# Performance work log

Measured on AMD Instinct MI355X. Metric: run time of the kernel, lower is better.

## Reference

```python
import jax, jax.numpy as jnp
import numpy as np

H = 16   # heads
M = 4    # stride / number of sparse slices


def setup_inputs() -> dict:
    key = jax.random.key(0)
    ks = jax.random.split(key, 5)
    B, L, D = 4, 4096, 1024
    s = 0.02
    return {
        "x": jax.random.normal(ks[0], (B, L, D), dtype=jnp.float32),
        "Wq": jax.random.normal(ks[1], (D, D), dtype=jnp.float32) * s,
        "bq": jnp.zeros((D,), dtype=jnp.float32),
        "Wk": jax.random.normal(ks[2], (D, D), dtype=jnp.float32) * s,
        "bk": jnp.zeros((D,), dtype=jnp.float32),
        "Wv": jax.random.normal(ks[3], (D, D), dtype=jnp.float32) * s,
        "bv": jnp.zeros((D,), dtype=jnp.float32),
        "Wo": jax.random.normal(ks[4], (D, D), dtype=jnp.float32) * s,
        "bo": jnp.zeros((D,), dtype=jnp.float32),
    }


def _strided_heads(y, B, L, D):
    # y: [B, L, D] -> [B, H, M, n, d_k] where slice m holds tokens m, m+M, m+2M, ...
    dk = D // H
    n = L // M
    y = y.reshape(B, L, H, dk).transpose(0, 2, 1, 3)          # [B,H,L,dk]
    y = y.reshape(B, H, n, M, dk).transpose(0, 1, 3, 2, 4)    # [B,H,M,n,dk]
    return y


def reference(x, Wq, bq, Wk, bk, Wv, bv, Wo, bo):
    B, L, D = x.shape
    dk = D // H
    n = L // M
    # projections (PyTorch Linear math: x @ W + b with W stored as [in, out] here)
    q = _strided_heads(x @ Wq + bq, B, L, D)   # [B,H,M,n,dk]
    k = _strided_heads(x @ Wk + bk, B, L, D)
    v = _strided_heads(x @ Wv + bv, B, L, D)
    # per-slice attention over the n strided tokens of each of the M slices
    scores = jnp.einsum("bhmqd,bhmkd->bhmqk", q, k) / jnp.sqrt(jnp.float32(dk))
    p = jax.nn.softmax(scores, axis=-1)
    o = jnp.einsum("bhmqk,bhmkd->bhmqd", p, v)                # [B,H,M,n,dk]
    # scatter back: slice m writes positions m::M  ==  interleave m and n dims
    o = o.transpose(0, 1, 3, 2, 4).reshape(B, H, L, dk)       # [B,H,L,dk]
    o = o.transpose(0, 2, 1, 3).reshape(B, L, D)              # [B,L,D]
    return o @ Wo + bo
```

## Files before the change

kernel.cpp:

```cpp
#include <hip/hip_runtime.h>
#include <hip/hip_bf16.h>


typedef __attribute__((ext_vector_type(8))) short short8;
typedef __attribute__((ext_vector_type(8))) unsigned short ushort8v;
typedef __attribute__((ext_vector_type(4))) float floatx4;

__device__ __forceinline__ float b2f(unsigned short h) {
    union { unsigned int u; float f; } v; v.u = ((unsigned int)h) << 16; return v.f;
}
__device__ __forceinline__ unsigned short f2b(float f) {
    union { float f; unsigned int u; } v; v.f = f;
    unsigned int r = v.u + 0x7fffu + ((v.u >> 16) & 1u);
    return (unsigned short)(r >> 16);
}
__device__ __forceinline__ unsigned int pack2bf(float lo, float hi) {
    union { float f; unsigned int u; } a, b; a.f = lo; b.f = hi;
    return ((b.u + 0x8000u) & 0xFFFF0000u) | (((a.u + 0x8000u) >> 16) & 0xFFFFu);
}
__device__ __forceinline__ void async_copy16(const unsigned short* g, unsigned short* l) {
    __builtin_amdgcn_global_load_lds((const __attribute__((address_space(1))) void*)g,
                                     (__attribute__((address_space(3))) void*)l, 16, 0, 0);
}

__global__ __launch_bounds__(256)
void cvt_kernel(const float* __restrict__ in, unsigned short* __restrict__ out, int n4) {
    int i = blockIdx.x * 256 + threadIdx.x;
    if (i >= n4) return;
    float4 v = ((const float4*)in)[i];
    ushort4 o;
    o.x = f2b(v.x); o.y = f2b(v.y); o.z = f2b(v.z); o.w = f2b(v.w);
    ((ushort4*)out)[i] = o;
}

__global__ __launch_bounds__(256)
void cvt_w_t(const float* __restrict__ Wq, const float* __restrict__ Wk,
             const float* __restrict__ Wv, const float* __restrict__ Wo,
             unsigned short* __restrict__ Wt3, unsigned short* __restrict__ Wot, float s0) {
    __shared__ float tile[64][65];
    const int kt = blockIdx.x, nt = blockIdx.y, z = blockIdx.z;
    const float* W = (z == 0) ? Wq : (z == 1) ? Wk : (z == 2) ? Wv : Wo;
    unsigned short* Wt = (z < 3) ? (Wt3 + (size_t)z * 1048576) : Wot;
    const float sc = (z == 0) ? s0 : 1.0f;
    const int t = threadIdx.x;
    const int r = t >> 2, cg = t & 3;
    const float* src = W + (size_t)(kt * 64 + r) * 1024 + nt * 64 + cg * 16;
#pragma unroll
    for (int j = 0; j < 4; j++) {
        float4 v = *(const float4*)(src + j * 4);
        tile[r][cg * 16 + j * 4 + 0] = v.x;
        tile[r][cg * 16 + j * 4 + 1] = v.y;
        tile[r][cg * 16 + j * 4 + 2] = v.z;
        tile[r][cg * 16 + j * 4 + 3] = v.w;
    }
    __syncthreads();
    unsigned short* dst = Wt + (size_t)(nt * 64 + r) * 1024 + kt * 64 + cg * 16;
    ushort8v o0, o1;
#pragma unroll
    for (int j = 0; j < 8; j++) o0[j] = f2b(tile[cg * 16 + j][r] * sc);
#pragma unroll
    for (int j = 0; j < 8; j++) o1[j] = f2b(tile[cg * 16 + 8 + j][r] * sc);
    *(ushort8v*)(dst) = o0;
    *(ushort8v*)(dst + 8) = o1;
}

template <bool F32OUT>
__global__ __launch_bounds__(256, 2)
void gemm_k(const unsigned short* __restrict__ A,
            const unsigned short* __restrict__ BtBase,
            const float* __restrict__ bias0,
            const float* __restrict__ bias1,
            const float* __restrict__ bias2,
            void* __restrict__ OutBase, float s0) {
    constexpr int K = 1024, N = 1024;
    __shared__ __align__(16) unsigned short As[256 * 64];
    __shared__ __align__(16) unsigned short Bs[128 * 64];
    const int id = blockIdx.x;
    const int xcd = id & 7;
    const int q = id >> 3;
    const int tileM = xcd * 8 + (q & 7);
    const int rz = q >> 3;
    const int tileN = rz & 7;
    const int z = rz >> 3;
    const unsigned short* Bt = BtBase + (size_t)z * (1024 * 1024);
    const float* bias = (z == 0) ? bias0 : (z == 1 ? bias1 : bias2);
    const float bs = (z == 0) ? s0 : 1.0f;
    const int tid = threadIdx.x, w = tid >> 6, lane = tid & 63;
    const int wr = w >> 1, wc = w & 1;
    const int g = lane >> 4, c = lane & 15;
    const int c7 = c & 7;
    const int r8 = lane >> 3, j8 = lane & 7;
    const int kcs = (j8 ^ r8) * 8;

    floatx4 acc[8][4];
#pragma unroll
    for (int i = 0; i < 8; i++)
#pragma unroll
        for (int jj = 0; jj < 4; jj++) acc[i][jj] = (floatx4){0.f, 0.f, 0.f, 0.f};

    for (int kt = 0; kt < K / 64; ++kt) {
        __syncthreads();
#pragma unroll
        for (int t = 0; t < 8; t++) {
            int seg = w * 8 + t;
            int rowA = tileM * 256 + seg * 8 + r8;
            async_copy16(A + (size_t)rowA * K + kt * 64 + kcs, As + seg * 512);
        }
#pragma unroll
        for (int t = 0; t < 4; t++) {
            int seg = w * 4 + t;
            int rowB = tileN * 128 + seg * 8 + r8;
            async_copy16(Bt + (size_t)rowB * K + kt * 64 + kcs, Bs + seg * 512);
        }
        __syncthreads();
#pragma unroll
        for (int ks = 0; ks < 2; ks++) {
            const int kx = ((ks * 4 + g) ^ c7) * 8;
            short8 bf[4];
#pragma unroll
            for (int ct = 0; ct < 4; ct++)
                bf[ct] = *(const short8*)(Bs + (wc * 64 + ct * 16 + c) * 64 + kx);
#pragma unroll
            for (int rt = 0; rt < 8; rt++) {
                short8 af = *(const short8*)(As + (wr * 128 + rt * 16 + c) * 64 + kx);
#pragma unroll
                for (int ct = 0; ct < 4; ct++)
                    acc[rt][ct] = __builtin_amdgcn_mfma_f32_16x16x32_bf16(af, bf[ct], acc[rt][ct], 0, 0, 0);
            }
        }
    }
#pragma unroll
    for (int ct = 0; ct < 4; ct++) {
        int col = tileN * 128 + wc * 64 + ct * 16 + c;
        float bvv = bias[col] * bs;
#pragma unroll
        for (int rt = 0; rt < 8; rt++) {
            int row0 = tileM * 256 + wr * 128 + rt * 16 + g * 4;
#pragma unroll
            for (int r = 0; r < 4; r++) {
                float v = acc[rt][ct][r] + bvv;
                if (F32OUT) {
                    ((float*)OutBase)[(size_t)(row0 + r) * N + col] = v;
                } else {
                    ((unsigned short*)OutBase)[(size_t)z * (16384ull * 1024ull) +
                                               (size_t)(row0 + r) * N + col] = f2b(v);
                }
            }
        }
    }
}

__global__ __launch_bounds__(256)
void vtrans(const unsigned short* __restrict__ V, unsigned short* __restrict__ Vt) {
    __shared__ unsigned short tile[64 * 72];
    const int it = blockIdx.x, s = blockIdx.y;
    const int m = s & 3, h = (s >> 2) & 15, b = s >> 6;
    const int tid = threadIdx.x;
    {
        int il = tid >> 2, cg = tid & 3;
        const unsigned short* gsrc =
            V + ((size_t)b * 4096 + m + 4 * (it * 64 + il)) * 1024 + h * 64 + cg * 16;
        *(ushort8v*)(tile + il * 72 + cg * 16) = *(const ushort8v*)gsrc;
        *(ushort8v*)(tile + il * 72 + cg * 16 + 8) = *(const ushort8v*)(gsrc + 8);
    }
    __syncthreads();
    {
        int dl = tid >> 2, ig = (tid & 3) * 16;
        ushort8v o0, o1;
#pragma unroll
        for (int j = 0; j < 8; j++) o0[j] = tile[(ig + j) * 72 + dl];
#pragma unroll
        for (int j = 0; j < 8; j++) o1[j] = tile[(ig + 8 + j) * 72 + dl];
        unsigned short* dst = Vt + (size_t)s * 65536 + (size_t)dl * 1024 + it * 64 + ig;
        *(ushort8v*)dst = o0;
        *(ushort8v*)(dst + 8) = o1;
    }
}

__global__ __launch_bounds__(256)
void attn_k(const unsigned short* __restrict__ Qg,
            const unsigned short* __restrict__ Kg,
            const unsigned short* __restrict__ Vt,
            unsigned short* __restrict__ Og) {
    __shared__ __align__(16) unsigned short Qs[128 * 64];
    __shared__ __align__(16) unsigned short Ks[64 * 64];
    __shared__ __align__(16) unsigned short Vs[64 * 64];
    __shared__ __align__(16) unsigned short Ps[4 * 2048];
    __shared__ float als[128];

    const int id = blockIdx.x;
    const int xcd = id & 7;
    const int qq = id >> 3;
    const int s = xcd * 32 + (qq >> 3);
    const int qt = qq & 7;
    const int m = s & 3, h = (s >> 2) & 15, b = s >> 6;
    const int tid = threadIdx.x, w = tid >> 6, lane = tid & 63;
    const int g = lane >> 4, c = lane & 15;
    const size_t rowBase = (size_t)b * 4096;
    const unsigned short* VtS = Vt + (size_t)s * 65536;

#pragma unroll
    for (int rt = 0; rt < 2; rt++)
#pragma unroll
        for (int ks = 0; ks < 2; ks++) {
            int token = m + 4 * (qt * 128 + w * 32 + rt * 16 + c);
            async_copy16(Qg + (rowBase + token) * 1024 + h * 64 + ks * 32 + g * 8,
                         Qs + ((w * 2 + rt) * 2 + ks) * 512);
        }

    floatx4 oacc[2][4];
#pragma unroll
    for (int rt = 0; rt < 2; rt++)
#pragma unroll
        for (int dt = 0; dt < 4; dt++) oacc[rt][dt] = (floatx4){0.f, 0.f, 0.f, 0.f};
    float lsum[2] = {0.f, 0.f};

    for (int kt = 0; kt < 16; ++kt) {
        __syncthreads();
#pragma unroll
        for (int ks = 0; ks < 2; ks++) {
            int token = m + 4 * (kt * 64 + w * 16 + c);
            async_copy16(Kg + (rowBase + token) * 1024 + h * 64 + ks * 32 + g * 8,
                         Ks + (w * 2 + ks) * 512);
        }
#pragma unroll
        for (int kc = 0; kc < 2; kc++) {
            async_copy16(VtS + (size_t)(w * 16 + c) * 1024 + kt * 64 + kc * 32 + g * 8,
                         Vs + (w * 2 + kc) * 512);
        }
        __syncthreads();

        floatx4 sacc[4][2];
#pragma unroll
        for (int k4 = 0; k4 < 4; k4++)
#pragma unroll
            for (int rt = 0; rt < 2; rt++) sacc[k4][rt] = (floatx4){0.f, 0.f, 0.f, 0.f};
#pragma unroll
        for (int ks = 0; ks < 2; ks++) {
            short8 kf[4], qf[2];
#pragma unroll
            for (int k4 = 0; k4 < 4; k4++)
                kf[k4] = *(const short8*)(Ks + (((k4 * 2 + ks) * 4 + g) * 16 + c) * 8);
#pragma unroll
            for (int rt = 0; rt < 2; rt++)
                qf[rt] = *(const short8*)(Qs + ((((w * 2 + rt) * 2 + ks) * 4 + g) * 16 + c) * 8);
#pragma unroll
            for (int k4 = 0; k4 < 4; k4++)
#pragma unroll
                for (int rt = 0; rt < 2; rt++)
                    sacc[k4][rt] = __builtin_amdgcn_mfma_f32_16x16x32_bf16(kf[k4], qf[rt], sacc[k4][rt], 0, 0, 0);
        }

#pragma unroll
        for (int k4 = 0; k4 < 4; k4++) {
            const int kc = k4 >> 1;
            const int gr = (k4 & 1) * 2 + (g >> 1);
            const int j0 = (g & 1) * 4;
#pragma unroll
            for (int rt = 0; rt < 2; rt++) {
                float e0 = __builtin_amdgcn_exp2f(sacc[k4][rt][0]);
                float e1 = __builtin_amdgcn_exp2f(sacc[k4][rt][1]);
                float e2 = __builtin_amdgcn_exp2f(sacc[k4][rt][2]);
                float e3 = __builtin_amdgcn_exp2f(sacc[k4][rt][3]);
                lsum[rt] += (e0 + e1) + (e2 + e3);
                uint2 pk;
                pk.x = pack2bf(e0, e1);
                pk.y = pack2bf(e2, e3);
                *(uint2*)(Ps + w * 2048 + (((rt * 2 + kc) * 4 + gr) * 16 + c) * 8 + j0) = pk;
            }
        }

#pragma unroll
        for (int kc = 0; kc < 2; kc++) {
            short8 pf[2], vf[4];
#pragma unroll
            for (int rt = 0; rt < 2; rt++)
                pf[rt] = *(const short8*)(Ps + w * 2048 + (((rt * 2 + kc) * 4 + g) * 16 + c) * 8);
#pragma unroll
            for (int dt = 0; dt < 4; dt++)
                vf[dt] = *(const short8*)(Vs + (((dt * 2 + kc) * 4 + g) * 16 + c) * 8);
#pragma unroll
            for (int rt = 0; rt < 2; rt++)
#pragma unroll
                for (int dt = 0; dt < 4; dt++)
                    oacc[rt][dt] = __builtin_amdgcn_mfma_f32_16x16x32_bf16(pf[rt], vf[dt], oacc[rt][dt], 0, 0, 0);
        }
    }

#pragma unroll
    for (int rt = 0; rt < 2; rt++) {
        float l = lsum[rt];
        l += __shfl_xor(l, 16, 64);
        l += __shfl_xor(l, 32, 64);
        if (lane < 16) als[w * 32 + rt * 16 + c] = 1.0f / l;
    }
    float4 li[2];
#pragma unroll
    for (int rt = 0; rt < 2; rt++) li[rt] = *(float4*)(&als[w * 32 + rt * 16 + g * 4]);

#pragma unroll
    for (int rt = 0; rt < 2; rt++) {
#pragma unroll
        for (int r = 0; r < 4; r++) {
            float inv = (r == 0) ? li[rt].x : (r == 1) ? li[rt].y : (r == 2) ? li[rt].z : li[rt].w;
            int token = m + 4 * (qt * 128 + w * 32 + rt * 16 + g * 4 + r);
            size_t rowOff = (rowBase + token) * 1024 + h * 64;
#pragma unroll
            for (int dt = 0; dt < 4; dt++)
                Og[rowOff + dt * 16 + c] = f2b(oacc[rt][dt][r] * inv);
        }
    }
}

extern "C" void kernel_launch(void* const* d_in, const int* in_sizes, int n_in,
                              void* d_out, int out_size, void* d_ws, size_t ws_size,
                              hipStream_t stream) {
    const float* x  = (const float*)d_in[0];
    const float* Wq = (const float*)d_in[1];
    const float* bq = (const float*)d_in[2];
    const float* Wk = (const float*)d_in[3];
    const float* bk = (const float*)d_in[4];
    const float* Wv = (const float*)d_in[5];
    const float* bv = (const float*)d_in[6];
    const float* Wo = (const float*)d_in[7];
    const float* bo = (const float*)d_in[8];

    const float SC = 0.18033688011112042f;

    char* ws = (char*)d_ws;
    const size_t SZ = 33554432;
    unsigned short* xb  = (unsigned short*)(ws);
    unsigned short* Vtp = (unsigned short*)(ws);
    unsigned short* qb  = (unsigned short*)(ws + SZ);
    unsigned short* ob  = (unsigned short*)(ws + 4 * SZ);
    unsigned short* Wt3 = (unsigned short*)(ws + 5 * SZ);
    unsigned short* Wot = Wt3 + 3ull * 1024 * 1024;

    cvt_kernel<<<16384, 256, 0, stream>>>(x, xb, 4194304);
    cvt_w_t<<<dim3(16, 16, 4), 256, 0, stream>>>(Wq, Wk, Wv, Wo, Wt3, Wot, SC);
    gemm_k<false><<<1536, 256, 0, stream>>>(xb, Wt3, bq, bk, bv, qb, SC);
    vtrans<<<dim3(16, 256), 256, 0, stream>>>(qb + 2ull * 16777216ull, Vtp);
    attn_k<<<2048, 256, 0, stream>>>(qb, qb + 16777216ull, Vtp, ob);
    gemm_k<true><<<512, 256, 0, stream>>>(ob, Wot, bo, bo, bo, d_out, 1.0f);
}
```

Before: 411.8 us.

## Keep Q in registers, compute softmax row sums via MFMA, raise occupancy

```diff
diff --git a/kernel.cpp b/kernel.cpp
--- a/kernel.cpp
+++ b/kernel.cpp
@@ -14,9 +14,8 @@
     unsigned int r = v.u + 0x7fffu + ((v.u >> 16) & 1u);
     return (unsigned short)(r >> 16);
 }
-__device__ __forceinline__ unsigned int pack2bf(float lo, float hi) {
-    union { float f; unsigned int u; } a, b; a.f = lo; b.f = hi;
-    return ((b.u + 0x8000u) & 0xFFFF0000u) | (((a.u + 0x8000u) >> 16) & 0xFFFFu);
+__device__ __forceinline__ unsigned int fbits(float f) {
+    union { float f; unsigned int u; } v; v.f = f; return v.u;
 }
 __device__ __forceinline__ void async_copy16(const unsigned short* g, unsigned short* l) {
     __builtin_amdgcn_global_load_lds((const __attribute__((address_space(1))) void*)g,
@@ -177,16 +176,14 @@
     }
 }
 
-__global__ __launch_bounds__(256)
+__global__ __launch_bounds__(256, 4)
 void attn_k(const unsigned short* __restrict__ Qg,
             const unsigned short* __restrict__ Kg,
             const unsigned short* __restrict__ Vt,
             unsigned short* __restrict__ Og) {
-    __shared__ __align__(16) unsigned short Qs[128 * 64];
     __shared__ __align__(16) unsigned short Ks[64 * 64];
     __shared__ __align__(16) unsigned short Vs[64 * 64];
     __shared__ __align__(16) unsigned short Ps[4 * 2048];
-    __shared__ float als[128];
 
     const int id = blockIdx.x;
     const int xcd = id & 7;
@@ -197,58 +194,59 @@
     const int tid = threadIdx.x, w = tid >> 6, lane = tid & 63;
     const int g = lane >> 4, c = lane & 15;
     const size_t rowBase = (size_t)b * 4096;
-    const unsigned short* VtS = Vt + (size_t)s * 65536;
-
+
+    short8 qf[2][2];
 #pragma unroll
     for (int rt = 0; rt < 2; rt++)
 #pragma unroll
-        for (int ks = 0; ks < 2; ks++) {
-            int token = m + 4 * (qt * 128 + w * 32 + rt * 16 + c);
-            async_copy16(Qg + (rowBase + token) * 1024 + h * 64 + ks * 32 + g * 8,
-                         Qs + ((w * 2 + rt) * 2 + ks) * 512);
-        }
-
-    floatx4 oacc[2][4];
-#pragma unroll
-    for (int rt = 0; rt < 2; rt++)
+        for (int ks = 0; ks < 2; ks++)
+            qf[rt][ks] = *(const short8*)(Qg +
+                (rowBase + (size_t)(m + 4 * (qt * 128 + w * 32 + rt * 16 + c))) * 1024 +
+                h * 64 + ks * 32 + g * 8);
+
+    const unsigned short* kPtr =
+        Kg + (rowBase + (size_t)(m + 4 * (w * 16 + c))) * 1024 + h * 64 + g * 8;
+    const unsigned short* vPtr =
+        Vt + (size_t)s * 65536 + (size_t)(w * 16 + c) * 1024 + g * 8;
+
+    short8 ones;
+#pragma unroll
+    for (int j = 0; j < 8; j++) ones[j] = (short)0x3F80;
+
+    floatx4 oacc[2][4], lacc[2];
+#pragma unroll
+    for (int rt = 0; rt < 2; rt++) {
+        lacc[rt] = (floatx4){0.f, 0.f, 0.f, 0.f};
 #pragma unroll
         for (int dt = 0; dt < 4; dt++) oacc[rt][dt] = (floatx4){0.f, 0.f, 0.f, 0.f};
-    float lsum[2] = {0.f, 0.f};
+    }
 
     for (int kt = 0; kt < 16; ++kt) {
         __syncthreads();
+        async_copy16(kPtr,      Ks + (w * 2 + 0) * 512);
+        async_copy16(kPtr + 32, Ks + (w * 2 + 1) * 512);
+        async_copy16(vPtr,      Vs + (w * 2 + 0) * 512);
+        async_copy16(vPtr + 32, Vs + (w * 2 + 1) * 512);
+        kPtr += 262144;
+        vPtr += 64;
+        __syncthreads();
+
+        floatx4 sacc[4][2];
+#pragma unroll
+        for (int k4 = 0; k4 < 4; k4++)
+#pragma unroll
+            for (int rt = 0; rt < 2; rt++) sacc[k4][rt] = (floatx4){0.f, 0.f, 0.f, 0.f};
 #pragma unroll
         for (int ks = 0; ks < 2; ks++) {
-            int token = m + 4 * (kt * 64 + w * 16 + c);
-            async_copy16(Kg + (rowBase + token) * 1024 + h * 64 + ks * 32 + g * 8,
-                         Ks + (w * 2 + ks) * 512);
-        }
-#pragma unroll
-        for (int kc = 0; kc < 2; kc++) {
-            async_copy16(VtS + (size_t)(w * 16 + c) * 1024 + kt * 64 + kc * 32 + g * 8,
-                         Vs + (w * 2 + kc) * 512);
-        }
-        __syncthreads();
-
-        floatx4 sacc[4][2];
-#pragma unroll
-        for (int k4 = 0; k4 < 4; k4++)
-#pragma unroll
-            for (int rt = 0; rt < 2; rt++) sacc[k4][rt] = (floatx4){0.f, 0.f, 0.f, 0.f};
-#pragma unroll
-        for (int ks = 0; ks < 2; ks++) {
-            short8 kf[4], qf[2];
+            short8 kf[4];
 #pragma unroll
             for (int k4 = 0; k4 < 4; k4++)
                 kf[k4] = *(const short8*)(Ks + (((k4 * 2 + ks) * 4 + g) * 16 + c) * 8);
 #pragma unroll
-            for (int rt = 0; rt < 2; rt++)
-                qf[rt] = *(const short8*)(Qs + ((((w * 2 + rt) * 2 + ks) * 4 + g) * 16 + c) * 8);
-#pragma unroll
             for (int k4 = 0; k4 < 4; k4++)
 #pragma unroll
                 for (int rt = 0; rt < 2; rt++)
-                    sacc[k4][rt] = __builtin_amdgcn_mfma_f32_16x16x32_bf16(kf[k4], qf[rt], sacc[k4][rt], 0, 0, 0);
+                    sacc[k4][rt] = __builtin_amdgcn_mfma_f32_16x16x32_bf16(kf[k4], qf[rt][ks], sacc[k4][rt], 0, 0, 0);
         }
 
 #pragma unroll
@@ -258,14 +256,13 @@
             const int j0 = (g & 1) * 4;
 #pragma unroll
             for (int rt = 0; rt < 2; rt++) {
-                float e0 = __builtin_amdgcn_exp2f(sacc[k4][rt][0]);
-                float e1 = __builtin_amdgcn_exp2f(sacc[k4][rt][1]);
-                float e2 = __builtin_amdgcn_exp2f(sacc[k4][rt][2]);
-                float e3 = __builtin_amdgcn_exp2f(sacc[k4][rt][3]);
-                lsum[rt] += (e0 + e1) + (e2 + e3);
+                unsigned int u0 = fbits(__builtin_amdgcn_exp2f(sacc[k4][rt][0])) + 0x8000u;
+                unsigned int u1 = fbits(__builtin_amdgcn_exp2f(sacc[k4][rt][1])) + 0x8000u;
+                unsigned int u2 = fbits(__builtin_amdgcn_exp2f(sacc[k4][rt][2])) + 0x8000u;
+                unsigned int u3 = fbits(__builtin_amdgcn_exp2f(sacc[k4][rt][3])) + 0x8000u;
                 uint2 pk;
-                pk.x = pack2bf(e0, e1);
-                pk.y = pack2bf(e2, e3);
+                pk.x = __builtin_amdgcn_perm(u1, u0, 0x07060302u);
+                pk.y = __builtin_amdgcn_perm(u3, u2, 0x07060302u);
                 *(uint2*)(Ps + w * 2048 + (((rt * 2 + kc) * 4 + gr) * 16 + c) * 8 + j0) = pk;
             }
         }
@@ -280,29 +277,20 @@
             for (int dt = 0; dt < 4; dt++)
                 vf[dt] = *(const short8*)(Vs + (((dt * 2 + kc) * 4 + g) * 16 + c) * 8);
 #pragma unroll
-            for (int rt = 0; rt < 2; rt++)
+            for (int rt = 0; rt < 2; rt++) {
+                lacc[rt] = __builtin_amdgcn_mfma_f32_16x16x32_bf16(pf[rt], ones, lacc[rt], 0, 0, 0);
 #pragma unroll
                 for (int dt = 0; dt < 4; dt++)
                     oacc[rt][dt] = __builtin_amdgcn_mfma_f32_16x16x32_bf16(pf[rt], vf[dt], oacc[rt][dt], 0, 0, 0);
+            }
         }
     }
 
 #pragma unroll
     for (int rt = 0; rt < 2; rt++) {
-        float l = lsum[rt];
-        l += __shfl_xor(l, 16, 64);
-        l += __shfl_xor(l, 32, 64);
-        if (lane < 16) als[w * 32 + rt * 16 + c] = 1.0f / l;
-    }
-    float4 li[2];
-#pragma unroll
-    for (int rt = 0; rt < 2; rt++) li[rt] = *(float4*)(&als[w * 32 + rt * 16 + g * 4]);
-
-#pragma unroll
-    for (int rt = 0; rt < 2; rt++) {
 #pragma unroll
         for (int r = 0; r < 4; r++) {
-            float inv = (r == 0) ? li[rt].x : (r == 1) ? li[rt].y : (r == 2) ? li[rt].z : li[rt].w;
+            float inv = 1.0f / lacc[rt][r];
             int token = m + 4 * (qt * 128 + w * 32 + rt * 16 + g * 4 + r);
             size_t rowOff = (rowBase + token) * 1024 + h * 64;
 #pragma unroll
```

Measured after the change: 391.7 us. 4.9% less time.
